# Performance work log

Hardware: AMD Instinct MI355X
Metric: run time of the kernel (lower is better)

The kernel has to match this reference:

```python
import jax, jax.numpy as jnp
import numpy as np

L, C, F, K = 8192, 2048, 128, 257  # timesteps, input_size, filter_size, lag (odd => symmetric 'same' pad)
NY = 256  # number of overwritten channel rows


def setup_inputs() -> dict:
    key = jax.random.key(0)
    k1, k2, k3, k4 = jax.random.split(key, 4)
    x = jax.random.normal(k1, (L, C), dtype=jnp.float32)
    Yt = jax.random.randint(k2, (NY,), 0, C)
    # learned parameters (torch.rand -> uniform[0,1))
    g = jax.random.uniform(k3, (C, F), dtype=jnp.float32)
    kernel = jax.random.uniform(k4, (F, K), dtype=jnp.float32)
    return {"x": x, "Yt": Yt, "g": g, "kernel": kernel}


def reference(x, Yt, g, kernel):
    # synapse[c] is the per-channel 1D filter; the original builds a dense
    # (C, C, K) kernel whose only non-zero slices are the diagonal, so the
    # full conv1d is mathematically a depthwise (grouped) conv.
    synapse = jnp.matmul(g, kernel)          # (C, K)
    lhs = x.T[None]                          # (1, C, L)  NCH
    rhs = synapse[:, None, :]                # (C, 1, K)  OIH, groups=C
    pad = (kernel.shape[1] - 1) // 2         # torch padding='same', odd K
    out = jax.lax.conv_general_dilated(
        lhs, rhs,
        window_strides=(1,),
        padding=[(pad, pad)],
        feature_group_count=x.shape[1],
        dimension_numbers=("NCH", "OIH", "NCH"),
    )                                        # (1, C, L)
    # result[:, Yt, :] = x.T[Yt] : scatter-overwrite selected channel rows
    out = out.at[:, Yt, :].set(x.T[Yt][None])
    return out
```

## Files before the change

kernel.cpp:

```cpp
#include <hip/hip_runtime.h>

#define LL   8192
#define CC   2048
#define FF   128
#define KK   257
#define PAD  128

#define SROWP 328
#define NT   18
#define NCH  4
#define NW   4
#define ROWS 1288

typedef __bf16 bf16x8 __attribute__((ext_vector_type(8)));
typedef float  f32x16 __attribute__((ext_vector_type(16)));

static __device__ __forceinline__ unsigned short f2bf(float f) {
    unsigned u = __float_as_uint(f);
    u = (u + 0x7fffu + ((u >> 16) & 1u)) >> 16;
    return (unsigned short)u;
}

__global__ __launch_bounds__(256) void synb_kernel(const float* __restrict__ g,
                                                   const float* __restrict__ kern,
                                                   const int* __restrict__ Yt, int ny,
                                                   unsigned short* __restrict__ synEb) {
    __shared__ int sfl[4];
    const int c0 = blockIdx.x * 4;
    const int t  = threadIdx.x;
    if (t < 4) sfl[t] = 0;
    __syncthreads();
    for (int i = t; i < ny; i += 256) {
        int y = Yt[i];
        #pragma unroll
        for (int ii = 0; ii < 4; ++ii) if (y == c0 + ii) sfl[ii] = 1;
    }
    __syncthreads();
    const float* g0 = g + (size_t)(c0 + 0) * FF;
    const float* g1 = g + (size_t)(c0 + 1) * FF;
    const float* g2 = g + (size_t)(c0 + 2) * FF;
    const float* g3 = g + (size_t)(c0 + 3) * FF;
    const int fl0 = sfl[0], fl1 = sfl[1], fl2 = sfl[2], fl3 = sfl[3];
    for (int p = t; p < SROWP; p += 256) {
        const int kk = p - 32;
        float a0 = 0.f, a1 = 0.f, a2 = 0.f, a3 = 0.f;
        const bool inr = (kk >= 0) && (kk < KK);
        if (inr) {
            #pragma unroll 8
            for (int f = 0; f < FF; ++f) {
                float kv = kern[f * KK + kk];
                a0 += kv * g0[f];
                a1 += kv * g1[f];
                a2 += kv * g2[f];
                a3 += kv * g3[f];
            }
        }
        float dlt = (kk == PAD) ? 1.f : 0.f;
        float v0 = inr ? (fl0 ? dlt : a0) : 0.f;
        float v1 = inr ? (fl1 ? dlt : a1) : 0.f;
        float v2 = inr ? (fl2 ? dlt : a2) : 0.f;
        float v3 = inr ? (fl3 ? dlt : a3) : 0.f;
        synEb[(size_t)(c0 + 0) * SROWP + p] = f2bf(v0);
        synEb[(size_t)(c0 + 1) * SROWP + p] = f2bf(v1);
        synEb[(size_t)(c0 + 2) * SROWP + p] = f2bf(v2);
        synEb[(size_t)(c0 + 3) * SROWP + p] = f2bf(v3);
    }
}

static __device__ __forceinline__ void stage_issue(const float* __restrict__ x,
                                                   int W0, int c0, int t,
                                                   float2* ev, float2* ov) {
    #pragma unroll
    for (int k = 0; k < 5; ++k) {
        int pidx = (k << 8) + t;
        int ch2  = pidx & 1;
        int pp   = pidx >> 1;
        int lg   = W0 + (pp << 1) - 128;
        const float* sp = x + (size_t)lg * CC + c0 + (ch2 << 1);
        float2 a = make_float2(0.f, 0.f);
        float2 b = make_float2(0.f, 0.f);
        if ((unsigned)lg       < (unsigned)LL) a = *(const float2*)sp;
        if ((unsigned)(lg + 1) < (unsigned)LL) b = *(const float2*)(sp + CC);
        ev[k] = a; ov[k] = b;
    }
}

static __device__ __forceinline__ void stage_write(unsigned short (*buf)[ROWS], int t,
                                                   const float2* ev, const float2* ov) {
    #pragma unroll
    for (int k = 0; k < 5; ++k) {
        int pidx = (k << 8) + t;
        int ch2  = pidx & 1;
        int pp   = pidx >> 1;
        int gq   = pp >> 2;
        int gp   = gq ^ ((gq >> 3) & 7);
        int dw   = (gp << 2) | (pp & 3);
        const float* pe = (const float*)&ev[k];
        const float* po = (const float*)&ov[k];
        #pragma unroll
        for (int c2 = 0; c2 < 2; ++c2) {
            unsigned val = (unsigned)f2bf(pe[c2]) | ((unsigned)f2bf(po[c2]) << 16);
            ((unsigned*)buf[(ch2 << 1) + c2])[dw] = val;
        }
    }
}

__global__ __launch_bounds__(256, 4) void fused_conv(const float* __restrict__ x,
                                                     const unsigned short* __restrict__ synEb,
                                                     float* __restrict__ out) {
    __shared__ alignas(16) unsigned short xch[2][NCH][ROWS];
    __shared__ alignas(16) unsigned short synD[NCH][2][SROWP];
    const int t = threadIdx.x;

    const int d  = blockIdx.x;
    const int cg = ((d & 7) << 6) | (d >> 4);
    const int c0 = cg << 2;
    const int L0 = ((d >> 3) & 1) << 12;

    const int ci = t >> 6;
    const int ln = t & 63;
    const int j = ln & 31, q = ln >> 5;
    const int gb = (j << 2) + q;
    const int ib   = (q << 3) - j + 32;
    const int ppar = ib & 1;
    const int e0   = (ib - ppar) >> 1;

    float2 ev[5], ov[5];
    stage_issue(x, L0, c0, t, ev, ov);

    for (int u = t; u < NCH * 2 * SROWP; u += 256) {
        int ci2 = u / (2 * SROWP);
        int rem = u - ci2 * (2 * SROWP);
        int p   = (rem >= SROWP) ? 1 : 0;
        int idx = rem - (p ? SROWP : 0);
        int src = idx + p;
        if (src > SROWP - 1) src = SROWP - 1;
        synD[ci2][p][idx] = synEb[(size_t)(c0 + ci2) * SROWP + src];
    }

    stage_write(xch[0], t, ev, ov);
    __syncthreads();

    const unsigned* bp = (const unsigned*)(synD[ci][ppar]) + e0;

    for (int w = 0; w < NW; ++w) {
        const int cur = w & 1;
        const int W0  = L0 + (w << 10);
        if (w + 1 < NW) stage_issue(x, W0 + 1024, c0, t, ev, ov);

        const char* xrow = (const char*)xch[cur][ci];
        f32x16 acc;
        #pragma unroll
        for (int r = 0; r < 16; ++r) acc[r] = 0.f;
        #pragma unroll
        for (int m = 0; m < NT; ++m) {
            int gq2 = gb + (m << 1);
            int gp2 = gq2 ^ ((gq2 >> 3) & 7);
            union { int4 i4; bf16x8 v; } A;
            A.i4 = *(const int4*)(xrow + (gp2 << 4));
            union { unsigned dd[4]; bf16x8 v; } B;
            B.dd[0] = bp[(m << 3) + 0];
            B.dd[1] = bp[(m << 3) + 1];
            B.dd[2] = bp[(m << 3) + 2];
            B.dd[3] = bp[(m << 3) + 3];
            acc = __builtin_amdgcn_mfma_f32_32x32x16_bf16(A.v, B.v, acc, 0, 0, 0);
        }
        float* o = out + (size_t)(c0 + ci) * LL + W0 + j;
        #pragma unroll
        for (int r = 0; r < 16; ++r) {
            int row = (r & 3) + ((r >> 2) << 3) + (q << 2);
            o[row << 5] = acc[r];
        }
        __syncthreads();
        if (w + 1 < NW) stage_write(xch[cur ^ 1], t, ev, ov);
        __syncthreads();
    }
}

extern "C" void kernel_launch(void* const* d_in, const int* in_sizes, int n_in,
                              void* d_out, int out_size, void* d_ws, size_t ws_size,
                              hipStream_t stream) {
    const float* x    = (const float*)d_in[0];
    const int*   Yt   = (const int*)  d_in[1];
    const float* g    = (const float*)d_in[2];
    const float* kern = (const float*)d_in[3];
    float* out = (float*)d_out;
    const int ny = in_sizes[1];

    unsigned short* synEb = (unsigned short*)d_ws;

    synb_kernel<<<CC / 4, 256, 0, stream>>>(g, kern, Yt, ny, synEb);
    fused_conv<<<1024, 256, 0, stream>>>(x, synEb, out);
}
```

Measured before the change: 164.8 us.

## Switch conv tiles to 16x16x32 MFMA with register-cached filter fragments

The Toeplitz-style MFMA conv now uses 16x16x32 bf16 MFMA with four accumulators per wave instead of one 32x32x16 MFMA chain, so it needs 9 K-steps instead of 18. The filter B fragments are loaded once into registers and reused across all windows rather than re-read from LDS every step. Staging now loads float4 (all four channels) per timestep pair and writes LDS directly, and one barrier per window is dropped. The price is more registers for the held fragments, and global load latency is no longer overlapped with the MFMA loop.

```diff
diff --git a/kernel.cpp b/kernel.cpp
--- a/kernel.cpp
+++ b/kernel.cpp
@@ -7,13 +7,13 @@
 #define PAD  128
 
 #define SROWP 328
-#define NT   18
+#define NT   9
 #define NCH  4
 #define NW   4
-#define ROWS 1288
+#define ROWS 1352
 
 typedef __bf16 bf16x8 __attribute__((ext_vector_type(8)));
-typedef float  f32x16 __attribute__((ext_vector_type(16)));
+typedef float  f32x4  __attribute__((ext_vector_type(4)));
 
 static __device__ __forceinline__ unsigned short f2bf(float f) {
     unsigned u = __float_as_uint(f);
@@ -67,40 +67,29 @@
     }
 }
 
-static __device__ __forceinline__ void stage_issue(const float* __restrict__ x,
-                                                   int W0, int c0, int t,
-                                                   float2* ev, float2* ov) {
+static __device__ __forceinline__ void stage(const float* __restrict__ x,
+                                             unsigned short (*buf)[ROWS],
+                                             int W0, int c0, int t) {
     #pragma unroll
-    for (int k = 0; k < 5; ++k) {
-        int pidx = (k << 8) + t;
-        int ch2  = pidx & 1;
-        int pp   = pidx >> 1;
-        int lg   = W0 + (pp << 1) - 128;
-        const float* sp = x + (size_t)lg * CC + c0 + (ch2 << 1);
-        float2 a = make_float2(0.f, 0.f);
-        float2 b = make_float2(0.f, 0.f);
-        if ((unsigned)lg       < (unsigned)LL) a = *(const float2*)sp;
-        if ((unsigned)(lg + 1) < (unsigned)LL) b = *(const float2*)(sp + CC);
-        ev[k] = a; ov[k] = b;
-    }
-}
-
-static __device__ __forceinline__ void stage_write(unsigned short (*buf)[ROWS], int t,
-                                                   const float2* ev, const float2* ov) {
-    #pragma unroll
-    for (int k = 0; k < 5; ++k) {
-        int pidx = (k << 8) + t;
-        int ch2  = pidx & 1;
-        int pp   = pidx >> 1;
-        int gq   = pp >> 2;
-        int gp   = gq ^ ((gq >> 3) & 7);
-        int dw   = (gp << 2) | (pp & 3);
-        const float* pe = (const float*)&ev[k];
-        const float* po = (const float*)&ov[k];
-        #pragma unroll
-        for (int c2 = 0; c2 < 2; ++c2) {
-            unsigned val = (unsigned)f2bf(pe[c2]) | ((unsigned)f2bf(po[c2]) << 16);
-            ((unsigned*)buf[(ch2 << 1) + c2])[dw] = val;
+    for (int k = 0; k < 3; ++k) {
+        int pp = (k << 8) + t;
+        if (pp < 672) {
+            int lg = W0 + (pp << 1) - 128;
+            const float* sp = x + (size_t)lg * CC + c0;
+            float4 a = make_float4(0.f, 0.f, 0.f, 0.f);
+            float4 b = make_float4(0.f, 0.f, 0.f, 0.f);
+            if ((unsigned)lg       < (unsigned)LL) a = *(const float4*)sp;
+            if ((unsigned)(lg + 1) < (unsigned)LL) b = *(const float4*)(sp + CC);
+            int gq = pp >> 2;
+            int gp = gq ^ ((gq >> 3) & 7);
+            int dw = (gp << 2) | (pp & 3);
+            const float* pe = (const float*)&a;
+            const float* po = (const float*)&b;
+            #pragma unroll
+            for (int c2 = 0; c2 < 4; ++c2) {
+                unsigned val = (unsigned)f2bf(pe[c2]) | ((unsigned)f2bf(po[c2]) << 16);
+                ((unsigned*)buf[c2])[dw] = val;
+            }
         }
     }
 }
@@ -119,14 +108,11 @@
 
     const int ci = t >> 6;
     const int ln = t & 63;
-    const int j = ln & 31, q = ln >> 5;
-    const int gb = (j << 2) + q;
-    const int ib   = (q << 3) - j + 32;
-    const int ppar = ib & 1;
-    const int e0   = (ib - ppar) >> 1;
-
-    float2 ev[5], ov[5];
-    stage_issue(x, L0, c0, t, ev, ov);
+    const int n  = ln & 15, q4 = ln >> 4;
+    const int gbase = (n << 1) + q4;
+    const int ib  = (q4 << 3) - n + 32;
+    const int par = ib & 1;
+    const int e0  = (ib - par) >> 1;
 
     for (int u = t; u < NCH * 2 * SROWP; u += 256) {
         int ci2 = u / (2 * SROWP);
@@ -137,42 +123,49 @@
         if (src > SROWP - 1) src = SROWP - 1;
         synD[ci2][p][idx] = synEb[(size_t)(c0 + ci2) * SROWP + src];
     }
-
-    stage_write(xch[0], t, ev, ov);
+    stage(x, xch[0], L0, c0, t);
     __syncthreads();
 
-    const unsigned* bp = (const unsigned*)(synD[ci][ppar]) + e0;
+    bf16x8 bfrag[NT];
+    {
+        const unsigned* bp = (const unsigned*)(synD[ci][par]) + e0;
+        #pragma unroll
+        for (int m = 0; m < NT; ++m) {
+            union { unsigned dd[4]; bf16x8 v; } B;
+            B.dd[0] = bp[(m << 4) + 0];
+            B.dd[1] = bp[(m << 4) + 1];
+            B.dd[2] = bp[(m << 4) + 2];
+            B.dd[3] = bp[(m << 4) + 3];
+            bfrag[m] = B.v;
+        }
+    }
 
     for (int w = 0; w < NW; ++w) {
         const int cur = w & 1;
         const int W0  = L0 + (w << 10);
-        if (w + 1 < NW) stage_issue(x, W0 + 1024, c0, t, ev, ov);
+        const char* xrow = (const char*)xch[cur][ci];
 
-        const char* xrow = (const char*)xch[cur][ci];
-        f32x16 acc;
+        f32x4 acc[4];
         #pragma unroll
-        for (int r = 0; r < 16; ++r) acc[r] = 0.f;
+        for (int s = 0; s < 4; ++s) acc[s] = (f32x4){0.f, 0.f, 0.f, 0.f};
         #pragma unroll
         for (int m = 0; m < NT; ++m) {
-            int gq2 = gb + (m << 1);
-            int gp2 = gq2 ^ ((gq2 >> 3) & 7);
-            union { int4 i4; bf16x8 v; } A;
-            A.i4 = *(const int4*)(xrow + (gp2 << 4));
-            union { unsigned dd[4]; bf16x8 v; } B;
-            B.dd[0] = bp[(m << 3) + 0];
-            B.dd[1] = bp[(m << 3) + 1];
-            B.dd[2] = bp[(m << 3) + 2];
-            B.dd[3] = bp[(m << 3) + 3];
-            acc = __builtin_amdgcn_mfma_f32_32x32x16_bf16(A.v, B.v, acc, 0, 0, 0);
+            #pragma unroll
+            for (int s = 0; s < 4; ++s) {
+                int g  = gbase + (s << 5) + (m << 2);
+                int gp = g ^ ((g >> 3) & 7);
+                union { int4 i4; bf16x8 v; } A;
+                A.i4 = *(const int4*)(xrow + (gp << 4));
+                acc[s] = __builtin_amdgcn_mfma_f32_16x16x32_bf16(A.v, bfrag[m], acc[s], 0, 0, 0);
+            }
         }
-        float* o = out + (size_t)(c0 + ci) * LL + W0 + j;
+        float* o = out + (size_t)(c0 + ci) * LL + W0 + (q4 << 6) + n;
         #pragma unroll
-        for (int r = 0; r < 16; ++r) {
-            int row = (r & 3) + ((r >> 2) << 3) + (q << 2);
-            o[row << 5] = acc[r];
+        for (int s = 0; s < 4; ++s) {
+            #pragma unroll
+            for (int r = 0; r < 4; ++r) o[(s << 8) + (r << 4)] = acc[s][r];
         }
-        __syncthreads();
-        if (w + 1 < NW) stage_write(xch[cur ^ 1], t, ev, ov);
+        if (w + 1 < NW) stage(x, xch[cur ^ 1], W0 + 1024, c0, t);
         __syncthreads();
     }
 }
```

After: 153.0 us. -7.1%, faster.
